# Performance work log

Measured on AMD Instinct MI355X. Metric: run time of the kernel, lower is better.

## Reference

```python
import jax, jax.numpy as jnp
import numpy as np

N_GRAPHS = 256
BN_EPS = 1e-5

def gcn_conv(x, row, col, W, b, n):
    # PyG GCNConv: add self-loops, symmetric deg^-1/2 normalization, scatter-add at col.
    deg = jnp.zeros((n,), x.dtype).at[col].add(1.0) + 1.0  # +1 for self-loop
    dinv = jax.lax.rsqrt(deg)
    xw = x @ W                                             # [N, H]
    msg = (dinv[row] * dinv[col])[:, None] * xw[row]       # [E, H] gathered messages
    agg = jnp.zeros_like(xw).at[col].add(msg)              # scatter-add to targets
    agg = agg + (dinv * dinv)[:, None] * xw                # self-loop contribution
    return agg + b

def batch_norm(x, gamma, beta):
    # BatchNorm1d over the node dimension (training-mode batch statistics)
    mu = jnp.mean(x, axis=0)
    var = jnp.var(x, axis=0)
    return (x - mu) * jax.lax.rsqrt(var + BN_EPS) * gamma + beta

def setup_inputs():
    key = jax.random.key(0)
    ks = jax.random.split(key, 8)
    N, F, H, C, E = 50000, 128, 128, 3, 1_600_000
    x = jax.random.normal(ks[0], (N, F), jnp.float32)
    edge_index = jax.random.randint(ks[1], (2, E), 0, N)
    batch = jnp.sort(jax.random.randint(ks[2], (N,), 0, N_GRAPHS))
    s = lambda k, sh, fan: jax.random.normal(k, sh, jnp.float32) / np.sqrt(fan).astype(np.float32)
    return {
        "x": x, "edge_index": edge_index, "batch": batch,
        "W1": s(ks[3], (F, H), F), "b1": jnp.zeros((H,), jnp.float32),
        "gamma1": jnp.ones((H,), jnp.float32), "beta1": jnp.zeros((H,), jnp.float32),
        "W2": s(ks[4], (H, H), H), "b2": jnp.zeros((H,), jnp.float32),
        "gamma2": jnp.ones((H,), jnp.float32), "beta2": jnp.zeros((H,), jnp.float32),
        "Wc": s(ks[5], (3 * H, C), 3 * H), "bc": jnp.zeros((C,), jnp.float32),
    }

def reference(x, edge_index, batch, W1, b1, gamma1, beta1, W2, b2, gamma2, beta2, Wc, bc):
    n = x.shape[0]
    row, col = edge_index[0], edge_index[1]
    h = jax.nn.relu(batch_norm(gcn_conv(x, row, col, W1, b1, n), gamma1, beta1))
    # dropout is identity in eval mode
    h = jax.nn.relu(batch_norm(gcn_conv(h, row, col, W2, b2, n), gamma2, beta2))
    cnt = jax.ops.segment_sum(jnp.ones((n,), h.dtype), batch, num_segments=N_GRAPHS)
    hsum = jax.ops.segment_sum(h, batch, num_segments=N_GRAPHS)
    hmean = hsum / jnp.maximum(cnt, 1.0)[:, None]
    hmax = jax.ops.segment_max(h, batch, num_segments=N_GRAPHS)
    hmax = jnp.where(cnt[:, None] > 0, hmax, 0.0)  # guard empty graphs
    g = jnp.concatenate([hmean, hmax, hsum], axis=1)  # [G, 3H]
    return g @ Wc + bc
```

## Files before the change

kernel.cpp:

```cpp
#include <hip/hip_runtime.h>

#define HF 128
#define TILE 128
#define CAP2 6144
#define NFINE_MAX 512
#define SORT_CHUNK 4096
#define BN_EPS 1e-5f

__device__ __forceinline__ unsigned short f2bf(float f) {
    unsigned u = __float_as_uint(f);
    unsigned rounding = 0x7FFF + ((u >> 16) & 1);
    return (unsigned short)((u + rounding) >> 16);
}

__global__ __launch_bounds__(256) void bucket_sort(const int* __restrict__ row,
                                                   const int* __restrict__ col,
                                                   unsigned* __restrict__ buckets,
                                                   int* __restrict__ cursor,
                                                   int E, int nfine) {
    __shared__ int hist[NFINE_MAX], lbase[NFINE_MAX], gbase[NFINE_MAX], lofs[NFINE_MAX];
    __shared__ int s[512];
    __shared__ unsigned staged[SORT_CHUNK];
    __shared__ unsigned short sbkt[SORT_CHUNK];
    int t = threadIdx.x;
    for (int i = t; i < NFINE_MAX; i += 256) { hist[i] = 0; lofs[i] = 0; }
    __syncthreads();
    int e0 = blockIdx.x * SORT_CHUNK;
    int n = min(SORT_CHUNK, E - e0);
    for (int i = t; i < n; i += 256) {
        int c = col[e0 + i];
        atomicAdd(&hist[c >> 7], 1);
    }
    __syncthreads();
    s[t] = hist[t];
    s[t + 256] = hist[t + 256];
    for (int o = 1; o < 512; o <<= 1) {
        __syncthreads();
        int idx = (t + 1) * (o << 1) - 1;
        if (idx < 512) s[idx] += s[idx - o];
    }
    __syncthreads();
    if (t == 0) s[511] = 0;
    for (int o = 256; o >= 1; o >>= 1) {
        __syncthreads();
        int idx = (t + 1) * (o << 1) - 1;
        if (idx < 512) { int tmp = s[idx - o]; s[idx - o] = s[idx]; s[idx] += tmp; }
    }
    __syncthreads();
    lbase[t] = s[t];
    lbase[t + 256] = s[t + 256];
    for (int b = t; b < nfine; b += 256) {
        int cnt = hist[b];
        gbase[b] = cnt ? atomicAdd(&cursor[b * 16], cnt) : 0;
    }
    __syncthreads();
    for (int i = t; i < n; i += 256) {
        int c = col[e0 + i];
        int r = row[e0 + i];
        int b = c >> 7;
        int pos = lbase[b] + atomicAdd(&lofs[b], 1);
        staged[pos] = ((unsigned)(c & 127) << 17) | (unsigned)r;
        sbkt[pos] = (unsigned short)b;
    }
    __syncthreads();
    for (int i = t; i < n; i += 256) {
        int b = sbkt[i];
        int pos = gbase[b] + (i - lbase[b]);
        if (pos < CAP2) buckets[(size_t)b * CAP2 + pos] = staged[i];
    }
}

__global__ __launch_bounds__(256) void tile_place2(const unsigned* __restrict__ buckets,
                                                   const int* __restrict__ cursor,
                                                   int* __restrict__ rowptr,
                                                   float* __restrict__ dinv,
                                                   int* __restrict__ srow,
                                                   const int* __restrict__ batch,
                                                   int* __restrict__ gstart,
                                                   int N, int NG, int nfine) {
    int b = blockIdx.x;
    int t = threadIdx.x;
    if (b < 2 && t < 129) {
        int g = b * 129 + t;
        if (g <= NG) {
            int lo = 0, hi = N;
            while (lo < hi) {
                int mid = (lo + hi) >> 1;
                if (batch[mid] < g) lo = mid + 1; else hi = mid;
            }
            gstart[g] = lo;
        }
    }
    __shared__ int h[TILE], loc[TILE], cur[TILE];
    __shared__ int red[256];
    __shared__ int stage[CAP2];
    int part = 0;
    for (int i = t; i < b; i += 256) part += min(cursor[i * 16], CAP2);
    red[t] = part;
    if (t < TILE) h[t] = 0;
    __syncthreads();
    for (int o = 128; o > 0; o >>= 1) {
        if (t < o) red[t] += red[t + o];
        __syncthreads();
    }
    int base = red[0];
    int sz = min(cursor[b * 16], CAP2);
    const unsigned* bk = buckets + (size_t)b * CAP2;
    for (int i = t; i < sz; i += 256) atomicAdd(&h[bk[i] >> 17], 1);
    __syncthreads();
    if (t < TILE) loc[t] = h[t];
    __syncthreads();
    for (int o = 1; o < TILE; o <<= 1) {
        int v = (t < TILE && t >= o) ? loc[t - o] : 0;
        __syncthreads();
        if (t < TILE) loc[t] += v;
        __syncthreads();
    }
    if (t < TILE) {
        int c = b * TILE + t;
        int excl = loc[t] - h[t];
        if (c < N) {
            rowptr[c] = base + excl;
            dinv[c] = rsqrtf((float)h[t] + 1.0f);
        }
        cur[t] = excl;
    }
    if (b == nfine - 1 && t == 0) rowptr[N] = base + sz;
    __syncthreads();
    for (int i = t; i < sz; i += 256) {
        unsigned p = bk[i];
        int pos = atomicAdd(&cur[p >> 17], 1);
        if (pos < CAP2) stage[pos] = (int)(p & 0x1FFFFu);
    }
    __syncthreads();
    for (int i = t; i < sz; i += 256) srow[base + i] = stage[i];
}

__global__ __launch_bounds__(256) void gemm_rt(const float* __restrict__ X,
                                               const float* __restrict__ W,
                                               unsigned short* __restrict__ Y,
                                               const float* __restrict__ ssum_in,
                                               const float* __restrict__ ssq_in,
                                               const float* __restrict__ gamma,
                                               const float* __restrict__ beta,
                                               const float* __restrict__ rowscale,
                                               float* __restrict__ ssum_zero,
                                               float* __restrict__ ssq_zero,
                                               int N, int applyBN) {
    __shared__ float xst[HF][68];
    int t = threadIdx.x;
    int row0 = blockIdx.x * 64;
    if (blockIdx.x == 0 && t < HF) { ssum_zero[t] = 0.f; ssq_zero[t] = 0.f; }
    {
        int f = t & 127;
        float sc = 1.0f, sh = 0.0f;
        if (applyBN) {
            float invn = 1.0f / (float)N;
            float mu = ssum_in[f] * invn;
            float var = ssq_in[f] * invn - mu * mu;
            sc = gamma[f] * rsqrtf(var + BN_EPS);
            sh = beta[f] - mu * sc;
        }
        for (int r = (t >> 7); r < 64; r += 2) {
            int rr = row0 + r;
            float v = (rr < N) ? X[(size_t)rr * HF + f] : 0.0f;
            if (applyBN) v = fmaxf(v * sc + sh, 0.0f);
            xst[f][r] = v;
        }
    }
    __syncthreads();
    int cg = t & 31;
    int rg = t >> 5;
    int r0 = rg * 8;
    float acc[8][4] = {};
    const float4* Wv = reinterpret_cast<const float4*>(W);
    #pragma unroll 2
    for (int f = 0; f < HF; ++f) {
        float4 w = Wv[f * 32 + cg];
        float4 x0 = *reinterpret_cast<const float4*>(&xst[f][r0]);
        float4 x1 = *reinterpret_cast<const float4*>(&xst[f][r0 + 4]);
        float xr[8] = {x0.x, x0.y, x0.z, x0.w, x1.x, x1.y, x1.z, x1.w};
        #pragma unroll
        for (int i = 0; i < 8; ++i) {
            acc[i][0] += xr[i] * w.x;
            acc[i][1] += xr[i] * w.y;
            acc[i][2] += xr[i] * w.z;
            acc[i][3] += xr[i] * w.w;
        }
    }
    #pragma unroll
    for (int i = 0; i < 8; ++i) {
        int rr = row0 + r0 + i;
        if (rr < N) {
            float rs = rowscale[rr];
            ushort4 o;
            o.x = f2bf(acc[i][0] * rs);
            o.y = f2bf(acc[i][1] * rs);
            o.z = f2bf(acc[i][2] * rs);
            o.w = f2bf(acc[i][3] * rs);
            *reinterpret_cast<ushort4*>(&Y[(size_t)rr * HF + cg * 4]) = o;
        }
    }
}

__global__ __launch_bounds__(256) void gather_conv(const int* __restrict__ rowptr,
                                                   const int* __restrict__ srow,
                                                   const float* __restrict__ dinv,
                                                   const unsigned short* __restrict__ XW,
                                                   const float* __restrict__ b,
                                                   float* __restrict__ OUT, int N) {
    int c = blockIdx.x * 16 + (threadIdx.x >> 4);
    int j = threadIdx.x & 15;
    if (c >= N) return;
    int e = rowptr[c], end = rowptr[c + 1];
    float acc[8] = {0.f, 0.f, 0.f, 0.f, 0.f, 0.f, 0.f, 0.f};
    const unsigned M = 0xffff0000u;
    for (; e + 3 < end; e += 4) {
        int r0 = srow[e], r1 = srow[e + 1], r2 = srow[e + 2], r3 = srow[e + 3];
        uint4 u0 = *reinterpret_cast<const uint4*>(XW + (size_t)r0 * HF + j * 8);
        uint4 u1 = *reinterpret_cast<const uint4*>(XW + (size_t)r1 * HF + j * 8);
        uint4 u2 = *reinterpret_cast<const uint4*>(XW + (size_t)r2 * HF + j * 8);
        uint4 u3 = *reinterpret_cast<const uint4*>(XW + (size_t)r3 * HF + j * 8);
        acc[0] += (__uint_as_float(u0.x << 16) + __uint_as_float(u1.x << 16))
                + (__uint_as_float(u2.x << 16) + __uint_as_float(u3.x << 16));
        acc[1] += (__uint_as_float(u0.x & M) + __uint_as_float(u1.x & M))
                + (__uint_as_float(u2.x & M) + __uint_as_float(u3.x & M));
        acc[2] += (__uint_as_float(u0.y << 16) + __uint_as_float(u1.y << 16))
                + (__uint_as_float(u2.y << 16) + __uint_as_float(u3.y << 16));
        acc[3] += (__uint_as_float(u0.y & M) + __uint_as_float(u1.y & M))
                + (__uint_as_float(u2.y & M) + __uint_as_float(u3.y & M));
        acc[4] += (__uint_as_float(u0.z << 16) + __uint_as_float(u1.z << 16))
                + (__uint_as_float(u2.z << 16) + __uint_as_float(u3.z << 16));
        acc[5] += (__uint_as_float(u0.z & M) + __uint_as_float(u1.z & M))
                + (__uint_as_float(u2.z & M) + __uint_as_float(u3.z & M));
        acc[6] += (__uint_as_float(u0.w << 16) + __uint_as_float(u1.w << 16))
                + (__uint_as_float(u2.w << 16) + __uint_as_float(u3.w << 16));
        acc[7] += (__uint_as_float(u0.w & M) + __uint_as_float(u1.w & M))
                + (__uint_as_float(u2.w & M) + __uint_as_float(u3.w & M));
    }
    for (; e < end; ++e) {
        int r0 = srow[e];
        uint4 u0 = *reinterpret_cast<const uint4*>(XW + (size_t)r0 * HF + j * 8);
        acc[0] += __uint_as_float(u0.x << 16);
        acc[1] += __uint_as_float(u0.x & M);
        acc[2] += __uint_as_float(u0.y << 16);
        acc[3] += __uint_as_float(u0.y & M);
        acc[4] += __uint_as_float(u0.z << 16);
        acc[5] += __uint_as_float(u0.z & M);
        acc[6] += __uint_as_float(u0.w << 16);
        acc[7] += __uint_as_float(u0.w & M);
    }
    float dc = dinv[c];
    uint4 xv = *reinterpret_cast<const uint4*>(XW + (size_t)c * HF + j * 8);
    acc[0] += __uint_as_float(xv.x << 16);
    acc[1] += __uint_as_float(xv.x & M);
    acc[2] += __uint_as_float(xv.y << 16);
    acc[3] += __uint_as_float(xv.y & M);
    acc[4] += __uint_as_float(xv.z << 16);
    acc[5] += __uint_as_float(xv.z & M);
    acc[6] += __uint_as_float(xv.w << 16);
    acc[7] += __uint_as_float(xv.w & M);
    float4 b0 = *reinterpret_cast<const float4*>(b + j * 8);
    float4 b1 = *reinterpret_cast<const float4*>(b + j * 8 + 4);
    float4 o0, o1;
    o0.x = dc * acc[0] + b0.x;
    o0.y = dc * acc[1] + b0.y;
    o0.z = dc * acc[2] + b0.z;
    o0.w = dc * acc[3] + b0.w;
    o1.x = dc * acc[4] + b1.x;
    o1.y = dc * acc[5] + b1.y;
    o1.z = dc * acc[6] + b1.z;
    o1.w = dc * acc[7] + b1.w;
    float* op = OUT + (size_t)c * HF + j * 8;
    *reinterpret_cast<float4*>(op) = o0;
    *reinterpret_cast<float4*>(op + 4) = o1;
}

__global__ __launch_bounds__(128) void bn_stats(const float* __restrict__ Y,
                                                float* __restrict__ ssum,
                                                float* __restrict__ ssq, int N) {
    int t = threadIdx.x;
    float s = 0.f, sq = 0.f;
    for (int n = blockIdx.x; n < N; n += gridDim.x) {
        float v = Y[(size_t)n * HF + t];
        s += v;
        sq += v * v;
    }
    atomicAdd(&ssum[t], s);
    atomicAdd(&ssq[t], sq);
}

__global__ __launch_bounds__(256) void pool_classify(const float* __restrict__ B,
                                                     const int* __restrict__ gstart,
                                                     const float* __restrict__ ssum,
                                                     const float* __restrict__ ssq,
                                                     const float* __restrict__ gamma,
                                                     const float* __restrict__ beta,
                                                     const float* __restrict__ Wc,
                                                     const float* __restrict__ bc,
                                                     float* __restrict__ out, int N) {
    int g = blockIdx.x;
    int t = threadIdx.x & 127;
    int half = threadIdx.x >> 7;
    int s0 = gstart[g], s1 = gstart[g + 1];
    float invn = 1.0f / (float)N;
    float mu = ssum[t] * invn;
    float var = ssq[t] * invn - mu * mu;
    float sc = gamma[t] * rsqrtf(var + BN_EPS);
    float sh = beta[t] - mu * sc;
    float sum = 0.f, mx = 0.f;
    for (int n = s0 + half; n < s1; n += 2) {
        float v = fmaxf(B[(size_t)n * HF + t] * sc + sh, 0.0f);
        sum += v;
        mx = fmaxf(mx, v);
    }
    __shared__ float shsum[2][HF], shmax[2][HF];
    __shared__ float red[3][HF];
    shsum[half][t] = sum;
    shmax[half][t] = mx;
    __syncthreads();
    if (half == 0) {
        sum += shsum[1][t];
        mx = fmaxf(mx, shmax[1][t]);
        float cntf = (float)(s1 - s0);
        float mean = sum / fmaxf(cntf, 1.0f);
        red[0][t] = mean * Wc[t * 3 + 0] + mx * Wc[(HF + t) * 3 + 0] + sum * Wc[(2 * HF + t) * 3 + 0];
        red[1][t] = mean * Wc[t * 3 + 1] + mx * Wc[(HF + t) * 3 + 1] + sum * Wc[(2 * HF + t) * 3 + 1];
        red[2][t] = mean * Wc[t * 3 + 2] + mx * Wc[(HF + t) * 3 + 2] + sum * Wc[(2 * HF + t) * 3 + 2];
    }
    __syncthreads();
    for (int o = 64; o > 0; o >>= 1) {
        if (half == 0 && t < o) {
            red[0][t] += red[0][t + o];
            red[1][t] += red[1][t + o];
            red[2][t] += red[2][t + o];
        }
        __syncthreads();
    }
    if (threadIdx.x < 3) out[g * 3 + threadIdx.x] = red[threadIdx.x][0] + bc[threadIdx.x];
}

extern "C" void kernel_launch(void* const* d_in, const int* in_sizes, int n_in,
                              void* d_out, int out_size, void* d_ws, size_t ws_size,
                              hipStream_t stream) {
    const float* x    = (const float*)d_in[0];
    const int*   ei   = (const int*)d_in[1];
    const int*   batch= (const int*)d_in[2];
    const float* W1   = (const float*)d_in[3];
    const float* b1   = (const float*)d_in[4];
    const float* g1   = (const float*)d_in[5];
    const float* be1  = (const float*)d_in[6];
    const float* W2   = (const float*)d_in[7];
    const float* b2   = (const float*)d_in[8];
    const float* g2   = (const float*)d_in[9];
    const float* be2  = (const float*)d_in[10];
    const float* Wc   = (const float*)d_in[11];
    const float* bc   = (const float*)d_in[12];
    float* out = (float*)d_out;

    const int N = in_sizes[0] / HF;
    const int E = in_sizes[1] / 2;
    const int NG = 256;
    const int* row = ei;
    const int* col = ei + E;
    const int total = N * HF;
    const int nfine = (N + TILE - 1) / TILE;

    char* w = (char*)d_ws;
    size_t off = 0;
    auto alloc = [&](size_t bytes) -> void* {
        void* p = w + off;
        off += (bytes + 255) & ~(size_t)255;
        return p;
    };
    int*            cursor    = (int*)alloc((size_t)nfine * 16 * 4);
    float*          dinv      = (float*)alloc((size_t)N * 4);
    int*            rowptr    = (int*)alloc(((size_t)N + 1) * 4);
    int*            gstart    = (int*)alloc((NG + 1) * 4);
    int*            srow      = (int*)alloc((size_t)E * 4);
    float*          ssum1     = (float*)alloc(HF * 4);
    float*          ssq1      = (float*)alloc(HF * 4);
    float*          ssum2     = (float*)alloc(HF * 4);
    float*          ssq2      = (float*)alloc(HF * 4);
    unsigned short* A         = (unsigned short*)alloc((size_t)total * 2);
    float*          B         = (float*)alloc((size_t)total * 4);
    unsigned*       buckets   = (unsigned*)A;

    const int T256 = 256;
    int gridGa   = (N + 15) / 16;
    int gridGemm = (N + 63) / 64;
    int gridSort = (E + SORT_CHUNK - 1) / SORT_CHUNK;

    hipMemsetAsync(cursor, 0, (size_t)nfine * 16 * 4, stream);
    bucket_sort<<<gridSort, T256, 0, stream>>>(row, col, buckets, cursor, E, nfine);
    tile_place2<<<nfine, T256, 0, stream>>>(buckets, cursor, rowptr, dinv, srow,
                                            batch, gstart, N, NG, nfine);

    gemm_rt<<<gridGemm, T256, 0, stream>>>(x, W1, A, nullptr, nullptr, nullptr, nullptr,
                                           dinv, ssum1, ssq1, N, 0);
    gather_conv<<<gridGa, T256, 0, stream>>>(rowptr, srow, dinv, A, b1, B, N);
    bn_stats<<<512, 128, 0, stream>>>(B, ssum1, ssq1, N);

    gemm_rt<<<gridGemm, T256, 0, stream>>>(B, W2, A, ssum1, ssq1, g1, be1,
                                           dinv, ssum2, ssq2, N, 1);
    gather_conv<<<gridGa, T256, 0, stream>>>(rowptr, srow, dinv, A, b2, B, N);
    bn_stats<<<512, 128, 0, stream>>>(B, ssum2, ssq2, N);

    pool_classify<<<NG, 256, 0, stream>>>(B, gstart, ssum2, ssq2, g2, be2, Wc, bc, out, N);
}
```

Before: 338.2 us.

## Fuse BN statistics into gather epilogue and store conv output as bf16

The gather_conv kernel now computes per-block partial sums and sums of squares of its outputs in shared memory, and a small bn_reduce kernel turns them into BN scale/shift. This replaces the separate bn_stats pass that reread the whole fp32 activation and used atomics. The conv output buffer is also stored in bf16 instead of fp32, which halves its write traffic and the reads in the next GEMM and in pooling. BN statistics are still taken from the fp32 values before rounding, but downstream consumers see bf16-rounded activations, so precision is slightly lower.

```diff
diff --git a/kernel.cpp b/kernel.cpp
--- a/kernel.cpp
+++ b/kernel.cpp
@@ -11,6 +11,12 @@
     unsigned u = __float_as_uint(f);
     unsigned rounding = 0x7FFF + ((u >> 16) & 1);
     return (unsigned short)((u + rounding) >> 16);
+}
+__device__ __forceinline__ float bf2f(unsigned short u) {
+    return __uint_as_float(((unsigned)u) << 16);
+}
+__device__ __forceinline__ unsigned packbf(float lo, float hi) {
+    return ((unsigned)f2bf(hi) << 16) | (unsigned)f2bf(lo);
 }
 
 __global__ __launch_bounds__(256) void bucket_sort(const int* __restrict__ row,
@@ -136,35 +142,32 @@
     for (int i = t; i < sz; i += 256) srow[base + i] = stage[i];
 }
 
-__global__ __launch_bounds__(256) void gemm_rt(const float* __restrict__ X,
+__global__ __launch_bounds__(256) void gemm_rt(const float* __restrict__ Xf,
+                                               const unsigned short* __restrict__ Xh,
                                                const float* __restrict__ W,
                                                unsigned short* __restrict__ Y,
-                                               const float* __restrict__ ssum_in,
-                                               const float* __restrict__ ssq_in,
-                                               const float* __restrict__ gamma,
-                                               const float* __restrict__ beta,
+                                               const float* __restrict__ scale,
+                                               const float* __restrict__ shift,
                                                const float* __restrict__ rowscale,
-                                               float* __restrict__ ssum_zero,
-                                               float* __restrict__ ssq_zero,
                                                int N, int applyBN) {
     __shared__ float xst[HF][68];
     int t = threadIdx.x;
     int row0 = blockIdx.x * 64;
-    if (blockIdx.x == 0 && t < HF) { ssum_zero[t] = 0.f; ssq_zero[t] = 0.f; }
     {
         int f = t & 127;
-        float sc = 1.0f, sh = 0.0f;
-        if (applyBN) {
-            float invn = 1.0f / (float)N;
-            float mu = ssum_in[f] * invn;
-            float var = ssq_in[f] * invn - mu * mu;
-            sc = gamma[f] * rsqrtf(var + BN_EPS);
-            sh = beta[f] - mu * sc;
-        }
+        float sc = applyBN ? scale[f] : 1.0f;
+        float sh = applyBN ? shift[f] : 0.0f;
         for (int r = (t >> 7); r < 64; r += 2) {
             int rr = row0 + r;
-            float v = (rr < N) ? X[(size_t)rr * HF + f] : 0.0f;
-            if (applyBN) v = fmaxf(v * sc + sh, 0.0f);
+            float v = 0.0f;
+            if (rr < N) {
+                if (applyBN) {
+                    v = bf2f(Xh[(size_t)rr * HF + f]);
+                    v = fmaxf(v * sc + sh, 0.0f);
+                } else {
+                    v = Xf[(size_t)rr * HF + f];
+                }
+            }
             xst[f][r] = v;
         }
     }
@@ -208,109 +211,148 @@
                                                    const float* __restrict__ dinv,
                                                    const unsigned short* __restrict__ XW,
                                                    const float* __restrict__ b,
-                                                   float* __restrict__ OUT, int N) {
-    int c = blockIdx.x * 16 + (threadIdx.x >> 4);
+                                                   unsigned short* __restrict__ OUT,
+                                                   float* __restrict__ psum,
+                                                   float* __restrict__ psq, int N) {
+    int blk = blockIdx.x;
+    int c = blk * 16 + (threadIdx.x >> 4);
     int j = threadIdx.x & 15;
-    if (c >= N) return;
-    int e = rowptr[c], end = rowptr[c + 1];
-    float acc[8] = {0.f, 0.f, 0.f, 0.f, 0.f, 0.f, 0.f, 0.f};
+    bool valid = (c < N);
     const unsigned M = 0xffff0000u;
-    for (; e + 3 < end; e += 4) {
-        int r0 = srow[e], r1 = srow[e + 1], r2 = srow[e + 2], r3 = srow[e + 3];
-        uint4 u0 = *reinterpret_cast<const uint4*>(XW + (size_t)r0 * HF + j * 8);
-        uint4 u1 = *reinterpret_cast<const uint4*>(XW + (size_t)r1 * HF + j * 8);
-        uint4 u2 = *reinterpret_cast<const uint4*>(XW + (size_t)r2 * HF + j * 8);
-        uint4 u3 = *reinterpret_cast<const uint4*>(XW + (size_t)r3 * HF + j * 8);
-        acc[0] += (__uint_as_float(u0.x << 16) + __uint_as_float(u1.x << 16))
-                + (__uint_as_float(u2.x << 16) + __uint_as_float(u3.x << 16));
-        acc[1] += (__uint_as_float(u0.x & M) + __uint_as_float(u1.x & M))
-                + (__uint_as_float(u2.x & M) + __uint_as_float(u3.x & M));
-        acc[2] += (__uint_as_float(u0.y << 16) + __uint_as_float(u1.y << 16))
-                + (__uint_as_float(u2.y << 16) + __uint_as_float(u3.y << 16));
-        acc[3] += (__uint_as_float(u0.y & M) + __uint_as_float(u1.y & M))
-                + (__uint_as_float(u2.y & M) + __uint_as_float(u3.y & M));
-        acc[4] += (__uint_as_float(u0.z << 16) + __uint_as_float(u1.z << 16))
-                + (__uint_as_float(u2.z << 16) + __uint_as_float(u3.z << 16));
-        acc[5] += (__uint_as_float(u0.z & M) + __uint_as_float(u1.z & M))
-                + (__uint_as_float(u2.z & M) + __uint_as_float(u3.z & M));
-        acc[6] += (__uint_as_float(u0.w << 16) + __uint_as_float(u1.w << 16))
-                + (__uint_as_float(u2.w << 16) + __uint_as_float(u3.w << 16));
-        acc[7] += (__uint_as_float(u0.w & M) + __uint_as_float(u1.w & M))
-                + (__uint_as_float(u2.w & M) + __uint_as_float(u3.w & M));
-    }
-    for (; e < end; ++e) {
-        int r0 = srow[e];
-        uint4 u0 = *reinterpret_cast<const uint4*>(XW + (size_t)r0 * HF + j * 8);
-        acc[0] += __uint_as_float(u0.x << 16);
-        acc[1] += __uint_as_float(u0.x & M);
-        acc[2] += __uint_as_float(u0.y << 16);
-        acc[3] += __uint_as_float(u0.y & M);
-        acc[4] += __uint_as_float(u0.z << 16);
-        acc[5] += __uint_as_float(u0.z & M);
-        acc[6] += __uint_as_float(u0.w << 16);
-        acc[7] += __uint_as_float(u0.w & M);
-    }
-    float dc = dinv[c];
-    uint4 xv = *reinterpret_cast<const uint4*>(XW + (size_t)c * HF + j * 8);
-    acc[0] += __uint_as_float(xv.x << 16);
-    acc[1] += __uint_as_float(xv.x & M);
-    acc[2] += __uint_as_float(xv.y << 16);
-    acc[3] += __uint_as_float(xv.y & M);
-    acc[4] += __uint_as_float(xv.z << 16);
-    acc[5] += __uint_as_float(xv.z & M);
-    acc[6] += __uint_as_float(xv.w << 16);
-    acc[7] += __uint_as_float(xv.w & M);
-    float4 b0 = *reinterpret_cast<const float4*>(b + j * 8);
-    float4 b1 = *reinterpret_cast<const float4*>(b + j * 8 + 4);
-    float4 o0, o1;
-    o0.x = dc * acc[0] + b0.x;
-    o0.y = dc * acc[1] + b0.y;
-    o0.z = dc * acc[2] + b0.z;
-    o0.w = dc * acc[3] + b0.w;
-    o1.x = dc * acc[4] + b1.x;
-    o1.y = dc * acc[5] + b1.y;
-    o1.z = dc * acc[6] + b1.z;
-    o1.w = dc * acc[7] + b1.w;
-    float* op = OUT + (size_t)c * HF + j * 8;
-    *reinterpret_cast<float4*>(op) = o0;
-    *reinterpret_cast<float4*>(op + 4) = o1;
-}
-
-__global__ __launch_bounds__(128) void bn_stats(const float* __restrict__ Y,
-                                                float* __restrict__ ssum,
-                                                float* __restrict__ ssq, int N) {
+    float o[8];
+    if (valid) {
+        int e = rowptr[c], end = rowptr[c + 1];
+        float acc[8] = {0.f, 0.f, 0.f, 0.f, 0.f, 0.f, 0.f, 0.f};
+        for (; e + 3 < end; e += 4) {
+            int r0 = srow[e], r1 = srow[e + 1], r2 = srow[e + 2], r3 = srow[e + 3];
+            uint4 u0 = *reinterpret_cast<const uint4*>(XW + (size_t)r0 * HF + j * 8);
+            uint4 u1 = *reinterpret_cast<const uint4*>(XW + (size_t)r1 * HF + j * 8);
+            uint4 u2 = *reinterpret_cast<const uint4*>(XW + (size_t)r2 * HF + j * 8);
+            uint4 u3 = *reinterpret_cast<const uint4*>(XW + (size_t)r3 * HF + j * 8);
+            acc[0] += (__uint_as_float(u0.x << 16) + __uint_as_float(u1.x << 16))
+                    + (__uint_as_float(u2.x << 16) + __uint_as_float(u3.x << 16));
+            acc[1] += (__uint_as_float(u0.x & M) + __uint_as_float(u1.x & M))
+                    + (__uint_as_float(u2.x & M) + __uint_as_float(u3.x & M));
+            acc[2] += (__uint_as_float(u0.y << 16) + __uint_as_float(u1.y << 16))
+                    + (__uint_as_float(u2.y << 16) + __uint_as_float(u3.y << 16));
+            acc[3] += (__uint_as_float(u0.y & M) + __uint_as_float(u1.y & M))
+                    + (__uint_as_float(u2.y & M) + __uint_as_float(u3.y & M));
+            acc[4] += (__uint_as_float(u0.z << 16) + __uint_as_float(u1.z << 16))
+                    + (__uint_as_float(u2.z << 16) + __uint_as_float(u3.z << 16));
+            acc[5] += (__uint_as_float(u0.z & M) + __uint_as_float(u1.z & M))
+                    + (__uint_as_float(u2.z & M) + __uint_as_float(u3.z & M));
+            acc[6] += (__uint_as_float(u0.w << 16) + __uint_as_float(u1.w << 16))
+                    + (__uint_as_float(u2.w << 16) + __uint_as_float(u3.w << 16));
+            acc[7] += (__uint_as_float(u0.w & M) + __uint_as_float(u1.w & M))
+                    + (__uint_as_float(u2.w & M) + __uint_as_float(u3.w & M));
+        }
+        for (; e < end; ++e) {
+            int r0 = srow[e];
+            uint4 u0 = *reinterpret_cast<const uint4*>(XW + (size_t)r0 * HF + j * 8);
+            acc[0] += __uint_as_float(u0.x << 16);
+            acc[1] += __uint_as_float(u0.x & M);
+            acc[2] += __uint_as_float(u0.y << 16);
+            acc[3] += __uint_as_float(u0.y & M);
+            acc[4] += __uint_as_float(u0.z << 16);
+            acc[5] += __uint_as_float(u0.z & M);
+            acc[6] += __uint_as_float(u0.w << 16);
+            acc[7] += __uint_as_float(u0.w & M);
+        }
+        float dc = dinv[c];
+        uint4 xv = *reinterpret_cast<const uint4*>(XW + (size_t)c * HF + j * 8);
+        acc[0] += __uint_as_float(xv.x << 16);
+        acc[1] += __uint_as_float(xv.x & M);
+        acc[2] += __uint_as_float(xv.y << 16);
+        acc[3] += __uint_as_float(xv.y & M);
+        acc[4] += __uint_as_float(xv.z << 16);
+        acc[5] += __uint_as_float(xv.z & M);
+        acc[6] += __uint_as_float(xv.w << 16);
+        acc[7] += __uint_as_float(xv.w & M);
+        float4 b0 = *reinterpret_cast<const float4*>(b + j * 8);
+        float4 b1 = *reinterpret_cast<const float4*>(b + j * 8 + 4);
+        float dcv = dc;
+        o[0] = dcv * acc[0] + b0.x;
+        o[1] = dcv * acc[1] + b0.y;
+        o[2] = dcv * acc[2] + b0.z;
+        o[3] = dcv * acc[3] + b0.w;
+        o[4] = dcv * acc[4] + b1.x;
+        o[5] = dcv * acc[5] + b1.y;
+        o[6] = dcv * acc[6] + b1.z;
+        o[7] = dcv * acc[7] + b1.w;
+        uint4 ov;
+        ov.x = packbf(o[0], o[1]);
+        ov.y = packbf(o[2], o[3]);
+        ov.z = packbf(o[4], o[5]);
+        ov.w = packbf(o[6], o[7]);
+        *reinterpret_cast<uint4*>(OUT + (size_t)c * HF + j * 8) = ov;
+    } else {
+        #pragma unroll
+        for (int k = 0; k < 8; ++k) o[k] = 0.f;
+    }
+    __shared__ float sval[16][HF + 4];
+    int r = threadIdx.x >> 4;
+    *reinterpret_cast<float4*>(&sval[r][j * 8]) = make_float4(o[0], o[1], o[2], o[3]);
+    *reinterpret_cast<float4*>(&sval[r][j * 8 + 4]) = make_float4(o[4], o[5], o[6], o[7]);
+    __syncthreads();
+    if (threadIdx.x < HF) {
+        float s = 0.f, sq = 0.f;
+        #pragma unroll
+        for (int rr = 0; rr < 16; ++rr) {
+            float v = sval[rr][threadIdx.x];
+            s += v;
+            sq += v * v;
+        }
+        psum[(size_t)blk * HF + threadIdx.x] = s;
+        psq[(size_t)blk * HF + threadIdx.x] = sq;
+    }
+}
+
+__global__ __launch_bounds__(256) void bn_reduce(const float* __restrict__ psum,
+                                                 const float* __restrict__ psq,
+                                                 const float* __restrict__ gamma,
+                                                 const float* __restrict__ beta,
+                                                 float* __restrict__ scale,
+                                                 float* __restrict__ shift,
+                                                 int nblk, int N) {
+    int f = blockIdx.x;
     int t = threadIdx.x;
     float s = 0.f, sq = 0.f;
-    for (int n = blockIdx.x; n < N; n += gridDim.x) {
-        float v = Y[(size_t)n * HF + t];
-        s += v;
-        sq += v * v;
-    }
-    atomicAdd(&ssum[t], s);
-    atomicAdd(&ssq[t], sq);
-}
-
-__global__ __launch_bounds__(256) void pool_classify(const float* __restrict__ B,
+    for (int i = t; i < nblk; i += 256) {
+        s += psum[(size_t)i * HF + f];
+        sq += psq[(size_t)i * HF + f];
+    }
+    __shared__ float ls[256], lq[256];
+    ls[t] = s; lq[t] = sq;
+    __syncthreads();
+    for (int o = 128; o > 0; o >>= 1) {
+        if (t < o) { ls[t] += ls[t + o]; lq[t] += lq[t + o]; }
+        __syncthreads();
+    }
+    if (t == 0) {
+        float invn = 1.0f / (float)N;
+        float mu = ls[0] * invn;
+        float var = lq[0] * invn - mu * mu;
+        float sc = gamma[f] * rsqrtf(var + BN_EPS);
+        scale[f] = sc;
+        shift[f] = beta[f] - mu * sc;
+    }
+}
+
+__global__ __launch_bounds__(256) void pool_classify(const unsigned short* __restrict__ Bh,
                                                      const int* __restrict__ gstart,
-                                                     const float* __restrict__ ssum,
-                                                     const float* __restrict__ ssq,
-                                                     const float* __restrict__ gamma,
-                                                     const float* __restrict__ beta,
+                                                     const float* __restrict__ scale,
+                                                     const float* __restrict__ shift,
                                                      const float* __restrict__ Wc,
                                                      const float* __restrict__ bc,
-                                                     float* __restrict__ out, int N) {
+                                                     float* __restrict__ out) {
     int g = blockIdx.x;
     int t = threadIdx.x & 127;
     int half = threadIdx.x >> 7;
     int s0 = gstart[g], s1 = gstart[g + 1];
-    float invn = 1.0f / (float)N;
-    float mu = ssum[t] * invn;
-    float var = ssq[t] * invn - mu * mu;
-    float sc = gamma[t] * rsqrtf(var + BN_EPS);
-    float sh = beta[t] - mu * sc;
+    float sc = scale[t], sh = shift[t];
     float sum = 0.f, mx = 0.f;
     for (int n = s0 + half; n < s1; n += 2) {
-        float v = fmaxf(B[(size_t)n * HF + t] * sc + sh, 0.0f);
+        float v = fmaxf(bf2f(Bh[(size_t)n * HF + t]) * sc + sh, 0.0f);
         sum += v;
         mx = fmaxf(mx, v);
     }
@@ -365,6 +407,7 @@
     const int* col = ei + E;
     const int total = N * HF;
     const int nfine = (N + TILE - 1) / TILE;
+    const int nblkGa = (N + 15) / 16;
 
     char* w = (char*)d_ws;
     size_t off = 0;
@@ -378,16 +421,15 @@
     int*            rowptr    = (int*)alloc(((size_t)N + 1) * 4);
     int*            gstart    = (int*)alloc((NG + 1) * 4);
     int*            srow      = (int*)alloc((size_t)E * 4);
-    float*          ssum1     = (float*)alloc(HF * 4);
-    float*          ssq1      = (float*)alloc(HF * 4);
-    float*          ssum2     = (float*)alloc(HF * 4);
-    float*          ssq2      = (float*)alloc(HF * 4);
+    float*          psum      = (float*)alloc((size_t)nblkGa * HF * 4);
+    float*          psq       = (float*)alloc((size_t)nblkGa * HF * 4);
+    float*          scale     = (float*)alloc(HF * 4);
+    float*          shift     = (float*)alloc(HF * 4);
     unsigned short* A         = (unsigned short*)alloc((size_t)total * 2);
-    float*          B         = (float*)alloc((size_t)total * 4);
+    unsigned short* B         = (unsigned short*)alloc((size_t)total * 2);
     unsigned*       buckets   = (unsigned*)A;
 
     const int T256 = 256;
-    int gridGa   = (N + 15) / 16;
     int gridGemm = (N + 63) / 64;
     int gridSort = (E + SORT_CHUNK - 1) / SORT_CHUNK;
 
@@ -396,15 +438,13 @@
     tile_place2<<<nfine, T256, 0, stream>>>(buckets, cursor, rowptr, dinv, srow,
                                             batch, gstart, N, NG, nfine);
 
-    gemm_rt<<<gridGemm, T256, 0, stream>>>(x, W1, A, nullptr, nullptr, nullptr, nullptr,
-                                           dinv, ssum1, ssq1, N, 0);
-    gather_conv<<<gridGa, T256, 0, stream>>>(rowptr, srow, dinv, A, b1, B, N);
-    bn_stats<<<512, 128, 0, stream>>>(B, ssum1, ssq1, N);
-
-    gemm_rt<<<gridGemm, T256, 0, stream>>>(B, W2, A, ssum1, ssq1, g1, be1,
-                                           dinv, ssum2, ssq2, N, 1);
-    gather_conv<<<gridGa, T256, 0, stream>>>(rowptr, srow, dinv, A, b2, B, N);
-    bn_stats<<<512, 128, 0, stream>>>(B, ssum2, ssq2, N);
-
-    pool_classify<<<NG, 256, 0, stream>>>(B, gstart, ssum2, ssq2, g2, be2, Wc, bc, out, N);
-}
+    gemm_rt<<<gridGemm, T256, 0, stream>>>(x, nullptr, W1, A, nullptr, nullptr, dinv, N, 0);
+    gather_conv<<<nblkGa, T256, 0, stream>>>(rowptr, srow, dinv, A, b1, B, psum, psq, N);
+    bn_reduce<<<HF, 256, 0, stream>>>(psum, psq, g1, be1, scale, shift, nblkGa, N);
+
+    gemm_rt<<<gridGemm, T256, 0, stream>>>(nullptr, B, W2, A, scale, shift, dinv, N, 1);
+    gather_conv<<<nblkGa, T256, 0, stream>>>(rowptr, srow, dinv, A, b2, B, psum, psq, N);
+    bn_reduce<<<HF, 256, 0, stream>>>(psum, psq, g2, be2, scale, shift, nblkGa, N);
+
+    pool_classify<<<NG, 256, 0, stream>>>(B, gstart, scale, shift, Wc, bc, out);
+}
```

Measured after the change: 288.4 us. 14.7% less time.
